# Kernel optimization log

Hardware: AMD Instinct MI355X
Metric: run time of the kernel (lower is better)

Reference implementation:

```python
import math
import jax, jax.numpy as jnp
import numpy as np

B, L, S, H, E, D = 4, 2048, 2048, 8, 64, 64

def setup_inputs() -> dict:
    key = jax.random.key(0)
    kq, kk, kv = jax.random.split(key, 3)
    return {
        "queries": jax.random.normal(kq, (B, L, H, E), dtype=jnp.float32),
        "keys": jax.random.normal(kk, (B, S, H, E), dtype=jnp.float32),
        "values": jax.random.normal(kv, (B, S, H, D), dtype=jnp.float32),
    }

def reference(queries, keys, values):
    E_ = queries.shape[-1]
    scale = 1.0 / math.sqrt(E_)
    # scores: [B, H, L, S]
    scores = jnp.einsum('blhe,bshe->bhls', queries, keys)
    A = jax.nn.softmax(scale * scores, axis=-1)
    # dropout omitted (eval mode / p=0.0)
    out = jnp.einsum('bhls,bshd->blhd', A, values)
    return out
```

## Files before the change

kernel.cpp:

```cpp
#include <hip/hip_runtime.h>
#include <hip/hip_bf16.h>


#define BNUM 4
#define LLEN 2048
#define SLEN 2048
#define HNUM 8
#define EDIM 64

typedef __attribute__((ext_vector_type(8))) short bf16x8;
typedef __attribute__((ext_vector_type(4))) float f32x4;

__device__ __forceinline__ short f2bf(float f) {
    union { __hip_bfloat16 b; short s; } u;
    u.b = __float2bfloat16(f);
    return u.s;
}

#if __has_builtin(__builtin_amdgcn_global_load_lds)
#define HAVE_GLL 1
#else
#define HAVE_GLL 0
#endif

__device__ __forceinline__ void stage16(const short* g, short* l) {
#if HAVE_GLL
    __builtin_amdgcn_global_load_lds(
        (const __attribute__((address_space(1))) void*)g,
        (__attribute__((address_space(3))) void*)l, 16, 0, 0);
#else
    *(bf16x8*)l = *(const bf16x8*)g;
#endif
}

__global__ __launch_bounds__(256)
void prep(const float* __restrict__ Kg, const float* __restrict__ Vg,
          short* __restrict__ Kc, short* __restrict__ Vt)
{
    __shared__ short tile[EDIM][80];
    if (blockIdx.y == 0) {
        const int t = blockIdx.x * 256 + threadIdx.x;
        const int e8 = t & 7;
        const int tmp = t >> 3;
        const int h = tmp & 7;
        const int tmp2 = tmp >> 3;
        const int s = tmp2 & (SLEN - 1);
        const int b = tmp2 >> 11;
        const float4* src = (const float4*)(Kg + (((size_t)(b * SLEN + s) * HNUM + h) * EDIM + e8 * 8));
        float4 a = src[0], bb = src[1];
        bf16x8 o;
        o[0]=f2bf(a.x);  o[1]=f2bf(a.y);  o[2]=f2bf(a.z);  o[3]=f2bf(a.w);
        o[4]=f2bf(bb.x); o[5]=f2bf(bb.y); o[6]=f2bf(bb.z); o[7]=f2bf(bb.w);
        *(bf16x8*)(Kc + ((size_t)((b * HNUM + h) * SLEN + s) * EDIM + e8 * 8)) = o;
    } else {
        if (blockIdx.x >= 1024) return;
        const int x = blockIdx.x;
        const int s0 = (x & 31) * 64;
        const int bh = x >> 5;
        const int b = bh >> 3, h = bh & 7;
        {
            const int sr = threadIdx.x >> 2, dc = (threadIdx.x & 3) * 16;
            const float4* src = (const float4*)(Vg + (((size_t)(b * SLEN + s0 + sr) * HNUM + h) * EDIM + dc));
            #pragma unroll
            for (int j4 = 0; j4 < 4; ++j4) {
                float4 a = src[j4];
                tile[dc + j4*4 + 0][sr] = f2bf(a.x);
                tile[dc + j4*4 + 1][sr] = f2bf(a.y);
                tile[dc + j4*4 + 2][sr] = f2bf(a.z);
                tile[dc + j4*4 + 3][sr] = f2bf(a.w);
            }
        }
        __syncthreads();
        {
            const int dr = threadIdx.x >> 2, sc = (threadIdx.x & 3) * 16;
            short* dst = Vt + ((size_t)((b * HNUM + h) * EDIM + dr) * SLEN + s0 + sc);
            *(bf16x8*)dst       = *(const bf16x8*)&tile[dr][sc];
            *(bf16x8*)(dst + 8) = *(const bf16x8*)&tile[dr][sc + 8];
        }
    }
}

__global__ __launch_bounds__(128, 2)
void fa_fwd(const float* __restrict__ Qg, const short* __restrict__ Kc,
            const short* __restrict__ Vt, float* __restrict__ Og)
{
    __shared__ short sKV[8704];
    __shared__ float sL[2][64];

    const int tid  = threadIdx.x;
    const int wave = tid >> 6;
    const int lane = tid & 63;
    const int m    = lane & 15;
    const int quad = lane >> 4;
    const int h = blockIdx.y, b = blockIdx.z;
    const int qbase = blockIdx.x * 64;
    const int bh = b * HNUM + h;

    const short* Kbh = Kc + (size_t)bh * SLEN * EDIM;
    const short* Vbh = Vt + (size_t)bh * EDIM * SLEN;

    const int l3 = lane >> 3;
    const int ksrcE = (wave * 32 + l3) * EDIM + ((lane & 7) ^ (l3 & 3)) * 8;
    const int ksrcO = (wave * 32 + l3) * EDIM + ((lane & 7) ^ (4 + (l3 & 3))) * 8;
    const int vsrcB = (lane >> 2) * SLEN + wave * 32 + ((lane & 3) ^ ((lane >> 2) & 3)) * 8;
    short* kdstB = sKV + (wave * 256 + lane) * 8;
    short* vdstB = sKV + 4096 + (wave * 256 + lane) * 8;

#define STAGE_TILE(s0)                                                        \
    do {                                                                      \
        _Pragma("unroll")                                                     \
        for (int p = 0; p < 4; ++p) {                                         \
            const int ks = ((p & 1) ? ksrcO : ksrcE) + (p >> 1) * 1024 + (p & 1) * 512; \
            stage16(Kbh + (size_t)(s0) * EDIM + ks, kdstB + p * 512);         \
            stage16(Vbh + (s0) + vsrcB + p * 16 * SLEN, vdstB + p * 512);     \
        }                                                                     \
    } while (0)

    const float csc = 0.18033688011112042f;
    bf16x8 qfrag[4][2];
    #pragma unroll
    for (int qt = 0; qt < 4; ++qt)
        #pragma unroll
        for (int kb = 0; kb < 2; ++kb) {
            const float* qp = Qg + ((size_t)(b * LLEN + qbase + qt * 16 + m) * HNUM + h) * EDIM
                              + kb * 32 + quad * 8;
            float4 x0 = *(const float4*)qp;
            float4 x1 = *(const float4*)(qp + 4);
            bf16x8 f;
            f[0]=f2bf(x0.x*csc); f[1]=f2bf(x0.y*csc); f[2]=f2bf(x0.z*csc); f[3]=f2bf(x0.w*csc);
            f[4]=f2bf(x1.x*csc); f[5]=f2bf(x1.y*csc); f[6]=f2bf(x1.z*csc); f[7]=f2bf(x1.w*csc);
            qfrag[qt][kb] = f;
        }

    const int gk  = ((m >> 2) & 1) * 4 + (m & 3);
    const int pi0 = 8 * (m >> 2) + (m & 3);
    const int kOff00 = (wave * 32 + pi0)     * 64 + ((quad)     ^ gk) * 8;
    const int kOff01 = (wave * 32 + pi0)     * 64 + ((4 + quad) ^ gk) * 8;
    const int kOff10 = (wave * 32 + pi0 + 4) * 64 + ((quad)     ^ gk) * 8;
    const int kOff11 = (wave * 32 + pi0 + 4) * 64 + ((4 + quad) ^ gk) * 8;
    const int vOffB  = 4096 + wave * 2048 + m * 32 + ((quad ^ (m & 3)) * 8);

    f32x4 oacc[4][4];
    #pragma unroll
    for (int i = 0; i < 4; ++i)
        #pragma unroll
        for (int j = 0; j < 4; ++j) oacc[i][j] = (f32x4){0.f, 0.f, 0.f, 0.f};
    float lsum[4] = {0.f, 0.f, 0.f, 0.f};

    STAGE_TILE(0);
    __syncthreads();

    for (int s0 = 0; s0 < SLEN; s0 += 64) {
        bf16x8 kf00 = *(const bf16x8*)(sKV + kOff00);
        bf16x8 kf01 = *(const bf16x8*)(sKV + kOff01);
        bf16x8 kf10 = *(const bf16x8*)(sKV + kOff10);
        bf16x8 kf11 = *(const bf16x8*)(sKV + kOff11);
        bf16x8 vf0 = *(const bf16x8*)(sKV + vOffB);
        bf16x8 vf1 = *(const bf16x8*)(sKV + vOffB + 512);
        bf16x8 vf2 = *(const bf16x8*)(sKV + vOffB + 1024);
        bf16x8 vf3 = *(const bf16x8*)(sKV + vOffB + 1536);

        __syncthreads();

        if (s0 + 64 < SLEN) STAGE_TILE(s0 + 64);

        #pragma unroll
        for (int qt = 0; qt < 4; ++qt) {
            f32x4 a0 = {0.f, 0.f, 0.f, 0.f};
            f32x4 a1 = {0.f, 0.f, 0.f, 0.f};
            a0 = __builtin_amdgcn_mfma_f32_16x16x32_bf16(kf00, qfrag[qt][0], a0, 0, 0, 0);
            a0 = __builtin_amdgcn_mfma_f32_16x16x32_bf16(kf01, qfrag[qt][1], a0, 0, 0, 0);
            a1 = __builtin_amdgcn_mfma_f32_16x16x32_bf16(kf10, qfrag[qt][0], a1, 0, 0, 0);
            a1 = __builtin_amdgcn_mfma_f32_16x16x32_bf16(kf11, qfrag[qt][1], a1, 0, 0, 0);
            float p0 = __builtin_amdgcn_exp2f(a0[0]);
            float p1 = __builtin_amdgcn_exp2f(a0[1]);
            float p2 = __builtin_amdgcn_exp2f(a0[2]);
            float p3 = __builtin_amdgcn_exp2f(a0[3]);
            float p4 = __builtin_amdgcn_exp2f(a1[0]);
            float p5 = __builtin_amdgcn_exp2f(a1[1]);
            float p6 = __builtin_amdgcn_exp2f(a1[2]);
            float p7 = __builtin_amdgcn_exp2f(a1[3]);
            lsum[qt] += ((p0 + p1) + (p2 + p3)) + ((p4 + p5) + (p6 + p7));
            bf16x8 pf;
            pf[0]=f2bf(p0); pf[1]=f2bf(p1); pf[2]=f2bf(p2); pf[3]=f2bf(p3);
            pf[4]=f2bf(p4); pf[5]=f2bf(p5); pf[6]=f2bf(p6); pf[7]=f2bf(p7);
            oacc[qt][0] = __builtin_amdgcn_mfma_f32_16x16x32_bf16(pf, vf0, oacc[qt][0], 0, 0, 0);
            oacc[qt][1] = __builtin_amdgcn_mfma_f32_16x16x32_bf16(pf, vf1, oacc[qt][1], 0, 0, 0);
            oacc[qt][2] = __builtin_amdgcn_mfma_f32_16x16x32_bf16(pf, vf2, oacc[qt][2], 0, 0, 0);
            oacc[qt][3] = __builtin_amdgcn_mfma_f32_16x16x32_bf16(pf, vf3, oacc[qt][3], 0, 0, 0);
        }

        __syncthreads();
    }

    #pragma unroll
    for (int qt = 0; qt < 4; ++qt) {
        float l = lsum[qt];
        l += __shfl_xor(l, 16);
        l += __shfl_xor(l, 32);
        if (lane < 16) sL[wave][qt * 16 + lane] = l;
    }
    __syncthreads();

    float* sO = (float*)sKV;
    if (wave == 0) {
        #pragma unroll
        for (int qt = 0; qt < 4; ++qt)
            #pragma unroll
            for (int dt = 0; dt < 4; ++dt)
                #pragma unroll
                for (int r = 0; r < 4; ++r)
                    sO[(qt * 16 + quad * 4 + r) * 68 + dt * 16 + m] = oacc[qt][dt][r];
    }
    __syncthreads();
    if (wave == 1) {
        #pragma unroll
        for (int qt = 0; qt < 4; ++qt)
            #pragma unroll
            for (int dt = 0; dt < 4; ++dt)
                #pragma unroll
                for (int r = 0; r < 4; ++r)
                    sO[(qt * 16 + quad * 4 + r) * 68 + dt * 16 + m] += oacc[qt][dt][r];
    }
    __syncthreads();

    {
        const int q = tid >> 1;
        const int dcol = (tid & 1) * 32;
        const float l = sL[0][q] + sL[1][q];
        const float inv = 1.0f / l;
        float* orow = Og + ((size_t)(b * LLEN + qbase + q) * HNUM + h) * EDIM + dcol;
        #pragma unroll
        for (int j = 0; j < 8; ++j) {
            float4 v = *(const float4*)(sO + q * 68 + dcol + j * 4);
            v.x *= inv; v.y *= inv; v.z *= inv; v.w *= inv;
            *(float4*)(orow + j * 4) = v;
        }
    }
}

extern "C" void kernel_launch(void* const* d_in, const int* in_sizes, int n_in,
                              void* d_out, int out_size, void* d_ws, size_t ws_size,
                              hipStream_t stream) {
    const float* Q = (const float*)d_in[0];
    const float* K = (const float*)d_in[1];
    const float* V = (const float*)d_in[2];
    float* O = (float*)d_out;

    const size_t NE = (size_t)BNUM * LLEN * HNUM * EDIM;
    short* Kc = (short*)d_ws;
    short* Vt = Kc + NE;

    prep<<<dim3(2048, 2), dim3(256), 0, stream>>>(K, V, Kc, Vt);
    fa_fwd<<<dim3(LLEN / 64, HNUM, BNUM), dim3(128), 0, stream>>>(Q, Kc, Vt, O);
}
```

Before: 140.7 us.

## Switch to fp16 MFMA with packed conversion, MFMA row sums, and block swizzle

Q, K, V and the probability tiles now use fp16 with packed round-toward-zero conversion instead of per-element bf16 rounding, and all MFMAs are the f16 variant. The row-sum of probabilities is computed with an extra MFMA against a ones vector instead of scalar adds and cross-lane shuffles. The grid is flattened to one dimension and remapped so consecutive blocks are spread across heads and batches, likely to balance L2 or XCD locality. The unnormalized exp values can overflow fp16 if scores are large, and the extra MFMA per q-tile adds matrix work.

```diff
diff --git a/kernel.cpp b/kernel.cpp
--- a/kernel.cpp
+++ b/kernel.cpp
@@ -8,13 +8,24 @@
 #define HNUM 8
 #define EDIM 64
 
-typedef __attribute__((ext_vector_type(8))) short bf16x8;
+typedef __attribute__((ext_vector_type(8))) short s16x8;
+typedef __attribute__((ext_vector_type(8))) _Float16 hf16x8;
+typedef __attribute__((ext_vector_type(2))) __fp16 fp16x2;
 typedef __attribute__((ext_vector_type(4))) float f32x4;
 
-__device__ __forceinline__ short f2bf(float f) {
-    union { __hip_bfloat16 b; short s; } u;
-    u.b = __float2bfloat16(f);
+__device__ __forceinline__ short f2h(float f) {
+    union { _Float16 h; short s; } u;
+    u.h = (_Float16)f;
     return u.s;
+}
+
+__device__ __forceinline__ s16x8 pk8(float4 a, float4 b) {
+    union { fp16x2 h[4]; s16x8 v; } u;
+    u.h[0] = __builtin_amdgcn_cvt_pkrtz(a.x, a.y);
+    u.h[1] = __builtin_amdgcn_cvt_pkrtz(a.z, a.w);
+    u.h[2] = __builtin_amdgcn_cvt_pkrtz(b.x, b.y);
+    u.h[3] = __builtin_amdgcn_cvt_pkrtz(b.z, b.w);
+    return u.v;
 }
 
 #if __has_builtin(__builtin_amdgcn_global_load_lds)
@@ -29,7 +40,7 @@
         (const __attribute__((address_space(1))) void*)g,
         (__attribute__((address_space(3))) void*)l, 16, 0, 0);
 #else
-    *(bf16x8*)l = *(const bf16x8*)g;
+    *(s16x8*)l = *(const s16x8*)g;
 #endif
 }
 
@@ -48,10 +59,7 @@
         const int b = tmp2 >> 11;
         const float4* src = (const float4*)(Kg + (((size_t)(b * SLEN + s) * HNUM + h) * EDIM + e8 * 8));
         float4 a = src[0], bb = src[1];
-        bf16x8 o;
-        o[0]=f2bf(a.x);  o[1]=f2bf(a.y);  o[2]=f2bf(a.z);  o[3]=f2bf(a.w);
-        o[4]=f2bf(bb.x); o[5]=f2bf(bb.y); o[6]=f2bf(bb.z); o[7]=f2bf(bb.w);
-        *(bf16x8*)(Kc + ((size_t)((b * HNUM + h) * SLEN + s) * EDIM + e8 * 8)) = o;
+        *(s16x8*)(Kc + ((size_t)((b * HNUM + h) * SLEN + s) * EDIM + e8 * 8)) = pk8(a, bb);
     } else {
         if (blockIdx.x >= 1024) return;
         const int x = blockIdx.x;
@@ -64,18 +72,18 @@
             #pragma unroll
             for (int j4 = 0; j4 < 4; ++j4) {
                 float4 a = src[j4];
-                tile[dc + j4*4 + 0][sr] = f2bf(a.x);
-                tile[dc + j4*4 + 1][sr] = f2bf(a.y);
-                tile[dc + j4*4 + 2][sr] = f2bf(a.z);
-                tile[dc + j4*4 + 3][sr] = f2bf(a.w);
+                tile[dc + j4*4 + 0][sr] = f2h(a.x);
+                tile[dc + j4*4 + 1][sr] = f2h(a.y);
+                tile[dc + j4*4 + 2][sr] = f2h(a.z);
+                tile[dc + j4*4 + 3][sr] = f2h(a.w);
             }
         }
         __syncthreads();
         {
             const int dr = threadIdx.x >> 2, sc = (threadIdx.x & 3) * 16;
             short* dst = Vt + ((size_t)((b * HNUM + h) * EDIM + dr) * SLEN + s0 + sc);
-            *(bf16x8*)dst       = *(const bf16x8*)&tile[dr][sc];
-            *(bf16x8*)(dst + 8) = *(const bf16x8*)&tile[dr][sc + 8];
+            *(s16x8*)dst       = *(const s16x8*)&tile[dr][sc];
+            *(s16x8*)(dst + 8) = *(const s16x8*)&tile[dr][sc + 8];
         }
     }
 }
@@ -92,8 +100,13 @@
     const int lane = tid & 63;
     const int m    = lane & 15;
     const int quad = lane >> 4;
-    const int h = blockIdx.y, b = blockIdx.z;
-    const int qbase = blockIdx.x * 64;
+
+    const int lin  = (int)blockIdx.x;
+    const int logi = ((lin & 7) << 7) + (lin >> 3);
+    const int qx = logi & 31;
+    const int h  = (logi >> 5) & 7;
+    const int b  = logi >> 8;
+    const int qbase = qx * 64;
     const int bh = b * HNUM + h;
 
     const short* Kbh = Kc + (size_t)bh * SLEN * EDIM;
@@ -117,7 +130,7 @@
     } while (0)
 
     const float csc = 0.18033688011112042f;
-    bf16x8 qfrag[4][2];
+    hf16x8 qfrag[4][2];
     #pragma unroll
     for (int qt = 0; qt < 4; ++qt)
         #pragma unroll
@@ -126,10 +139,11 @@
                               + kb * 32 + quad * 8;
             float4 x0 = *(const float4*)qp;
             float4 x1 = *(const float4*)(qp + 4);
-            bf16x8 f;
-            f[0]=f2bf(x0.x*csc); f[1]=f2bf(x0.y*csc); f[2]=f2bf(x0.z*csc); f[3]=f2bf(x0.w*csc);
-            f[4]=f2bf(x1.x*csc); f[5]=f2bf(x1.y*csc); f[6]=f2bf(x1.z*csc); f[7]=f2bf(x1.w*csc);
-            qfrag[qt][kb] = f;
+            float4 y0 = {x0.x*csc, x0.y*csc, x0.z*csc, x0.w*csc};
+            float4 y1 = {x1.x*csc, x1.y*csc, x1.z*csc, x1.w*csc};
+            union { s16x8 s; hf16x8 h; } u;
+            u.s = pk8(y0, y1);
+            qfrag[qt][kb] = u.h;
         }
 
     const int gk  = ((m >> 2) & 1) * 4 + (m & 3);
@@ -140,25 +154,31 @@
     const int kOff11 = (wave * 32 + pi0 + 4) * 64 + ((4 + quad) ^ gk) * 8;
     const int vOffB  = 4096 + wave * 2048 + m * 32 + ((quad ^ (m & 3)) * 8);
 
+    hf16x8 vones;
+    #pragma unroll
+    for (int j = 0; j < 8; ++j) vones[j] = (_Float16)1.0f;
+
     f32x4 oacc[4][4];
+    f32x4 lacc[4];
     #pragma unroll
-    for (int i = 0; i < 4; ++i)
+    for (int i = 0; i < 4; ++i) {
         #pragma unroll
         for (int j = 0; j < 4; ++j) oacc[i][j] = (f32x4){0.f, 0.f, 0.f, 0.f};
-    float lsum[4] = {0.f, 0.f, 0.f, 0.f};
+        lacc[i] = (f32x4){0.f, 0.f, 0.f, 0.f};
+    }
 
     STAGE_TILE(0);
     __syncthreads();
 
     for (int s0 = 0; s0 < SLEN; s0 += 64) {
-        bf16x8 kf00 = *(const bf16x8*)(sKV + kOff00);
-        bf16x8 kf01 = *(const bf16x8*)(sKV + kOff01);
-        bf16x8 kf10 = *(const bf16x8*)(sKV + kOff10);
-        bf16x8 kf11 = *(const bf16x8*)(sKV + kOff11);
-        bf16x8 vf0 = *(const bf16x8*)(sKV + vOffB);
-        bf16x8 vf1 = *(const bf16x8*)(sKV + vOffB + 512);
-        bf16x8 vf2 = *(const bf16x8*)(sKV + vOffB + 1024);
-        bf16x8 vf3 = *(const bf16x8*)(sKV + vOffB + 1536);
+        hf16x8 kf00 = *(const hf16x8*)(sKV + kOff00);
+        hf16x8 kf01 = *(const hf16x8*)(sKV + kOff01);
+        hf16x8 kf10 = *(const hf16x8*)(sKV + kOff10);
+        hf16x8 kf11 = *(const hf16x8*)(sKV + kOff11);
+        hf16x8 vf0 = *(const hf16x8*)(sKV + vOffB);
+        hf16x8 vf1 = *(const hf16x8*)(sKV + vOffB + 512);
+        hf16x8 vf2 = *(const hf16x8*)(sKV + vOffB + 1024);
+        hf16x8 vf3 = *(const hf16x8*)(sKV + vOffB + 1536);
 
         __syncthreads();
 
@@ -168,10 +188,10 @@
         for (int qt = 0; qt < 4; ++qt) {
             f32x4 a0 = {0.f, 0.f, 0.f, 0.f};
             f32x4 a1 = {0.f, 0.f, 0.f, 0.f};
-            a0 = __builtin_amdgcn_mfma_f32_16x16x32_bf16(kf00, qfrag[qt][0], a0, 0, 0, 0);
-            a0 = __builtin_amdgcn_mfma_f32_16x16x32_bf16(kf01, qfrag[qt][1], a0, 0, 0, 0);
-            a1 = __builtin_amdgcn_mfma_f32_16x16x32_bf16(kf10, qfrag[qt][0], a1, 0, 0, 0);
-            a1 = __builtin_amdgcn_mfma_f32_16x16x32_bf16(kf11, qfrag[qt][1], a1, 0, 0, 0);
+            a0 = __builtin_amdgcn_mfma_f32_16x16x32_f16(kf00, qfrag[qt][0], a0, 0, 0, 0);
+            a0 = __builtin_amdgcn_mfma_f32_16x16x32_f16(kf01, qfrag[qt][1], a0, 0, 0, 0);
+            a1 = __builtin_amdgcn_mfma_f32_16x16x32_f16(kf10, qfrag[qt][0], a1, 0, 0, 0);
+            a1 = __builtin_amdgcn_mfma_f32_16x16x32_f16(kf11, qfrag[qt][1], a1, 0, 0, 0);
             float p0 = __builtin_amdgcn_exp2f(a0[0]);
             float p1 = __builtin_amdgcn_exp2f(a0[1]);
             float p2 = __builtin_amdgcn_exp2f(a0[2]);
@@ -180,25 +200,28 @@
             float p5 = __builtin_amdgcn_exp2f(a1[1]);
             float p6 = __builtin_amdgcn_exp2f(a1[2]);
             float p7 = __builtin_amdgcn_exp2f(a1[3]);
-            lsum[qt] += ((p0 + p1) + (p2 + p3)) + ((p4 + p5) + (p6 + p7));
-            bf16x8 pf;
-            pf[0]=f2bf(p0); pf[1]=f2bf(p1); pf[2]=f2bf(p2); pf[3]=f2bf(p3);
-            pf[4]=f2bf(p4); pf[5]=f2bf(p5); pf[6]=f2bf(p6); pf[7]=f2bf(p7);
-            oacc[qt][0] = __builtin_amdgcn_mfma_f32_16x16x32_bf16(pf, vf0, oacc[qt][0], 0, 0, 0);
-            oacc[qt][1] = __builtin_amdgcn_mfma_f32_16x16x32_bf16(pf, vf1, oacc[qt][1], 0, 0, 0);
-            oacc[qt][2] = __builtin_amdgcn_mfma_f32_16x16x32_bf16(pf, vf2, oacc[qt][2], 0, 0, 0);
-            oacc[qt][3] = __builtin_amdgcn_mfma_f32_16x16x32_bf16(pf, vf3, oacc[qt][3], 0, 0, 0);
+            union { fp16x2 h2[4]; hf16x8 v; } pu;
+            pu.h2[0] = __builtin_amdgcn_cvt_pkrtz(p0, p1);
+            pu.h2[1] = __builtin_amdgcn_cvt_pkrtz(p2, p3);
+            pu.h2[2] = __builtin_amdgcn_cvt_pkrtz(p4, p5);
+            pu.h2[3] = __builtin_amdgcn_cvt_pkrtz(p6, p7);
+            hf16x8 pf = pu.v;
+            lacc[qt] = __builtin_amdgcn_mfma_f32_16x16x32_f16(pf, vones, lacc[qt], 0, 0, 0);
+            oacc[qt][0] = __builtin_amdgcn_mfma_f32_16x16x32_f16(pf, vf0, oacc[qt][0], 0, 0, 0);
+            oacc[qt][1] = __builtin_amdgcn_mfma_f32_16x16x32_f16(pf, vf1, oacc[qt][1], 0, 0, 0);
+            oacc[qt][2] = __builtin_amdgcn_mfma_f32_16x16x32_f16(pf, vf2, oacc[qt][2], 0, 0, 0);
+            oacc[qt][3] = __builtin_amdgcn_mfma_f32_16x16x32_f16(pf, vf3, oacc[qt][3], 0, 0, 0);
         }
 
         __syncthreads();
     }
 
-    #pragma unroll
-    for (int qt = 0; qt < 4; ++qt) {
-        float l = lsum[qt];
-        l += __shfl_xor(l, 16);
-        l += __shfl_xor(l, 32);
-        if (lane < 16) sL[wave][qt * 16 + lane] = l;
+    if (m == 0) {
+        #pragma unroll
+        for (int qt = 0; qt < 4; ++qt)
+            #pragma unroll
+            for (int r = 0; r < 4; ++r)
+                sL[wave][qt * 16 + quad * 4 + r] = lacc[qt][r];
     }
     __syncthreads();
 
@@ -252,5 +275,5 @@
     short* Vt = Kc + NE;
 
     prep<<<dim3(2048, 2), dim3(256), 0, stream>>>(K, V, Kc, Vt);
-    fa_fwd<<<dim3(LLEN / 64, HNUM, BNUM), dim3(128), 0, stream>>>(Q, Kc, Vt, O);
-}
+    fa_fwd<<<dim3(1024), dim3(128), 0, stream>>>(Q, Kc, Vt, O);
+}
```

New measurement: 137.2 us. 1.03x faster.
